# Optimization experiments

Measured on AMD Instinct MI355X. Metric: run time of the kernel, lower is better.

Reference implementation:

```python
import jax, jax.numpy as jnp
import numpy as np

def setup_inputs() -> dict:
    key = jax.random.key(0)
    k1, k2, k3, k4, k5 = jax.random.split(key, 5)
    vocab, embed, hidden = 32000, 1024, 1024
    batch, src_len = 64, 512
    src = jax.random.randint(k1, (batch, src_len), 0, vocab)
    emb_table = jax.random.normal(k2, (vocab, embed), dtype=jnp.float32)
    # xavier_uniform bounds
    bx = float(np.sqrt(6.0 / (embed + hidden)))
    bh = float(np.sqrt(6.0 / (hidden + hidden)))
    W_xh = jax.random.uniform(k3, (hidden, embed), minval=-bx, maxval=bx, dtype=jnp.float32)
    b_xh = jax.random.uniform(k4, (hidden,), minval=-1.0/np.sqrt(embed), maxval=1.0/np.sqrt(embed), dtype=jnp.float32)
    W_hh = jax.random.uniform(k5, (hidden, hidden), minval=-bh, maxval=bh, dtype=jnp.float32)
    return {"src": src, "emb_table": emb_table, "W_xh": W_xh, "b_xh": b_xh, "W_hh": W_hh}

def reference(src, emb_table, W_xh, b_xh, W_hh):
    # embedded: (batch, src_len, embed)
    embedded = emb_table[src]
    # precompute input projection for all timesteps: (batch, src_len, hidden)
    x_proj = jnp.einsum('bte,he->bth', embedded, W_xh) + b_xh
    batch = src.shape[0]
    hidden = W_hh.shape[0]
    h0 = jnp.zeros((batch, hidden), dtype=jnp.float32)

    def step(h, x_t):
        h_new = jnp.tanh(x_t + h @ W_hh.T)
        return h_new, None

    # scan over time: x_proj transposed to (src_len, batch, hidden)
    h_final, _ = jax.lax.scan(step, h0, jnp.swapaxes(x_proj, 0, 1))
    return h_final
```

## Files before the change

### kernel.cpp

```cpp
#include <hip/hip_runtime.h>
#include <hip/hip_fp16.h>

typedef _Float16 half8 __attribute__((ext_vector_type(8)));
typedef float floatx4 __attribute__((ext_vector_type(4)));

#define HBUF_BYTES (2ull * 16 * 1024 * 8)
#define CTL_BYTES  (32ull * 1024)
#define XP_OFF     (HBUF_BYTES + CTL_BYTES)
#define XP_BYTES   (512ull * 64 * 1024 * 2)

#define TAG_BIT    (1ull << 14)

union pack4 { unsigned long long u; _Float16 h[4]; };

__device__ inline half8 cvt8(const float4 a, const float4 b) {
    half8 r;
    r[0] = (_Float16)a.x; r[1] = (_Float16)a.y; r[2] = (_Float16)a.z; r[3] = (_Float16)a.w;
    r[4] = (_Float16)b.x; r[5] = (_Float16)b.y; r[6] = (_Float16)b.z; r[7] = (_Float16)b.w;
    return r;
}

__global__ __launch_bounds__(256) void xproj_kernel(
    const int* __restrict__ src, const float* __restrict__ emb,
    const float* __restrict__ Wxh, const float* __restrict__ bxh,
    _Float16* __restrict__ xp)
{
    __shared__ _Float16 As[128][40];
    __shared__ _Float16 Bs[128][40];

    const int tid  = threadIdx.x;
    const int lane = tid & 63;
    const int w    = tid >> 6;
    const int m15  = lane & 15;
    const int quad = lane >> 4;
    const int bid  = blockIdx.x;
    const int bn   = bid & 7;
    const int bm   = bid >> 3;
    const int m0   = bm * 128, n0 = bn * 128;
    const int wm   = w & 1, wn = w >> 1;

    const int  srow = tid >> 1;
    const int  scol = (tid & 1) * 16;
    const long arow = (long)src[m0 + srow] * 1024;
    const float* abase = emb + arow + scol;
    const float* bbase = Wxh + (long)(n0 + srow) * 1024 + scol;

    floatx4 zero4 = {0.f, 0.f, 0.f, 0.f};
    floatx4 acc[4][4];
#pragma unroll
    for (int mt = 0; mt < 4; mt++)
#pragma unroll
        for (int nt = 0; nt < 4; nt++) acc[mt][nt] = zero4;

    for (int k0 = 0; k0 < 1024; k0 += 32) {
        __syncthreads();
        float4 a0 = *(const float4*)(abase + k0);
        float4 a1 = *(const float4*)(abase + k0 + 4);
        float4 a2 = *(const float4*)(abase + k0 + 8);
        float4 a3 = *(const float4*)(abase + k0 + 12);
        float4 b0 = *(const float4*)(bbase + k0);
        float4 b1 = *(const float4*)(bbase + k0 + 4);
        float4 b2 = *(const float4*)(bbase + k0 + 8);
        float4 b3 = *(const float4*)(bbase + k0 + 12);
        *(half8*)&As[srow][scol]     = cvt8(a0, a1);
        *(half8*)&As[srow][scol + 8] = cvt8(a2, a3);
        *(half8*)&Bs[srow][scol]     = cvt8(b0, b1);
        *(half8*)&Bs[srow][scol + 8] = cvt8(b2, b3);
        __syncthreads();

        half8 af[4], bf[4];
#pragma unroll
        for (int mt = 0; mt < 4; mt++)
            af[mt] = *(const half8*)&As[wm * 64 + mt * 16 + m15][quad * 8];
#pragma unroll
        for (int nt = 0; nt < 4; nt++)
            bf[nt] = *(const half8*)&Bs[wn * 64 + nt * 16 + m15][quad * 8];
#pragma unroll
        for (int mt = 0; mt < 4; mt++)
#pragma unroll
            for (int nt = 0; nt < 4; nt++)
                acc[mt][nt] = __builtin_amdgcn_mfma_f32_16x16x32_f16(
                    af[mt], bf[nt], acc[mt][nt], 0, 0, 0);
    }

#pragma unroll
    for (int nt = 0; nt < 4; nt++) {
        const int n = n0 + wn * 64 + nt * 16 + m15;
        const float bias = bxh[n];
#pragma unroll
        for (int mt = 0; mt < 4; mt++) {
            const int mrow = m0 + wm * 64 + mt * 16 + quad * 4;
#pragma unroll
            for (int r = 0; r < 4; r++) {
                const int m = mrow + r;
                const int b = m >> 9;
                const int t = m & 511;
                xp[((long)t * 64 + b) * 1024 + n] = (_Float16)(acc[mt][nt][r] + bias);
            }
        }
    }
}

__global__ __launch_bounds__(256, 1) void rnn_kernel(
    const float* __restrict__ Whh, const _Float16* __restrict__ xp,
    unsigned long long* __restrict__ hb, float* __restrict__ out)
{
    __shared__ _Float16 hstage[16][1032];
    __shared__ floatx4  cred[4][4][64];

    const int tid    = threadIdx.x;
    const int lane   = tid & 63;
    const int w      = tid >> 6;
    const int m15    = lane & 15;
    const int quad   = lane >> 4;
    const int wg     = blockIdx.x;
    const int g      = wg & 15;
    const int member = wg >> 4;
    const int b0     = g * 4;

    for (int i = tid; i < 16 * 1032; i += 256) ((_Float16*)hstage)[i] = (_Float16)0.f;

    half8 Wf[4][8];
#pragma unroll
    for (int nt = 0; nt < 4; nt++) {
        const float* wrow = Whh + (long)(member * 64 + nt * 16 + m15) * 1024
                                + w * 256 + quad * 8;
#pragma unroll
        for (int kk = 0; kk < 8; kk++) {
            float4 lo = *(const float4*)(wrow + kk * 32);
            float4 hi = *(const float4*)(wrow + kk * 32 + 4);
            Wf[nt][kk] = cvt8(lo, hi);
        }
    }
    __syncthreads();

    const int dim = member * 64 + w * 16 + m15;
    float xv[4] = {0.f, 0.f, 0.f, 0.f};
    if (quad == 0) {
#pragma unroll
        for (int r = 0; r < 4; r++)
            xv[r] = (float)xp[((long)0 * 64 + b0 + r) * 1024 + dim];
    }

    floatx4 zero4 = {0.f, 0.f, 0.f, 0.f};

    for (int t = 0; t < 512; t++) {
        const unsigned long long* hcu = hb + (size_t)(t & 1) * 16384 + (size_t)g * 1024;
        unsigned long long*       hnu = hb + (size_t)((t + 1) & 1) * 16384 + (size_t)g * 1024;
        const unsigned long long exp_tag = (unsigned long long)(((t + 1) >> 1) & 1) << 14;

        unsigned long long v[4];
        for (;;) {
            bool ok = true;
#pragma unroll
            for (int i = 0; i < 4; i++)
                v[i] = __hip_atomic_load(hcu + tid + 256 * i, __ATOMIC_RELAXED,
                                         __HIP_MEMORY_SCOPE_AGENT);
#pragma unroll
            for (int i = 0; i < 4; i++)
                ok &= ((v[i] & TAG_BIT) == exp_tag);
            if (ok) break;
        }
#pragma unroll
        for (int i = 0; i < 4; i++) {
            pack4 p; p.u = v[i] & ~TAG_BIT;
            const int d = tid + 256 * i;
#pragma unroll
            for (int b = 0; b < 4; b++) hstage[b][d] = p.h[b];
        }
        __syncthreads();

        floatx4 pacc[4];
#pragma unroll
        for (int nt = 0; nt < 4; nt++) pacc[nt] = zero4;
#pragma unroll
        for (int kk = 0; kk < 8; kk++) {
            half8 a = *(const half8*)&hstage[m15][w * 256 + kk * 32 + quad * 8];
#pragma unroll
            for (int nt = 0; nt < 4; nt++)
                pacc[nt] = __builtin_amdgcn_mfma_f32_16x16x32_f16(
                    a, Wf[nt][kk], pacc[nt], 0, 0, 0);
        }

#pragma unroll
        for (int nt = 0; nt < 4; nt++) cred[w][nt][lane] = pacc[nt];
        __syncthreads();
        floatx4 dsum = cred[0][w][lane];
#pragma unroll
        for (int ww = 1; ww < 4; ww++) dsum += cred[ww][w][lane];

        if (quad == 0) {
            pack4 p;
#pragma unroll
            for (int r = 0; r < 4; r++) {
                float pre  = dsum[r] + xv[r];
                float e    = __expf(2.0f * pre);
                float hval = 1.0f - 2.0f / (e + 1.0f);
                p.h[r] = (_Float16)hval;
                if (t == 511) out[(b0 + r) * 1024 + dim] = hval;
            }
            if (t < 511) {
                const unsigned long long st_tag =
                    (unsigned long long)(((t + 2) >> 1) & 1) << 14;
                __hip_atomic_store(hnu + dim, p.u | st_tag, __ATOMIC_RELAXED,
                                   __HIP_MEMORY_SCOPE_AGENT);
            }
        }

        if (t < 511 && quad == 0) {
#pragma unroll
            for (int r = 0; r < 4; r++)
                xv[r] = (float)xp[((long)(t + 1) * 64 + b0 + r) * 1024 + dim];
        }
    }
}

extern "C" void kernel_launch(void* const* d_in, const int* in_sizes, int n_in,
                              void* d_out, int out_size, void* d_ws, size_t ws_size,
                              hipStream_t stream) {
    const int*   src = (const int*)d_in[0];
    const float* emb = (const float*)d_in[1];
    const float* Wxh = (const float*)d_in[2];
    const float* bxh = (const float*)d_in[3];
    const float* Whh = (const float*)d_in[4];
    float* out = (float*)d_out;

    char* ws = (char*)d_ws;
    unsigned long long* hb = (unsigned long long*)ws;
    _Float16* xp = (_Float16*)(ws + XP_OFF);

    hipMemsetAsync(ws, 0, HBUF_BYTES, stream);

    hipLaunchKernelGGL(xproj_kernel, dim3(2048), dim3(256), 0, stream,
                       src, emb, Wxh, bxh, xp);

    hipLaunchKernelGGL(rnn_kernel, dim3(256), dim3(256), 0, stream,
                       Whh, xp, hb, out);
}
```

Before: 1.197 ms.

## Give each wave full K per output tile, double-buffer h staging, drop cross-wave reduction

Each wave now owns one 16-column output tile and holds all 32 K-slices of W_hh in registers, so the per-step LDS cross-wave reduction and its extra barrier go away. The hidden-state staging buffer is double-buffered, and the poll for the next step's h moves to the end of the loop, cutting barriers to one per step. The poll also skips reloading entries already seen with the right tag. In exchange each wave carries more weight registers and runs a longer serial chain of MFMAs per step, split over two accumulators.

```diff
diff --git a/kernel.cpp b/kernel.cpp
--- a/kernel.cpp
+++ b/kernel.cpp
@@ -105,8 +105,7 @@
     const float* __restrict__ Whh, const _Float16* __restrict__ xp,
     unsigned long long* __restrict__ hb, float* __restrict__ out)
 {
-    __shared__ _Float16 hstage[16][1032];
-    __shared__ floatx4  cred[4][4][64];
+    __shared__ _Float16 hstage[2][16][1032];
 
     const int tid    = threadIdx.x;
     const int lane   = tid & 63;
@@ -118,18 +117,16 @@
     const int member = wg >> 4;
     const int b0     = g * 4;
 
-    for (int i = tid; i < 16 * 1032; i += 256) ((_Float16*)hstage)[i] = (_Float16)0.f;
-
-    half8 Wf[4][8];
-#pragma unroll
-    for (int nt = 0; nt < 4; nt++) {
-        const float* wrow = Whh + (long)(member * 64 + nt * 16 + m15) * 1024
-                                + w * 256 + quad * 8;
-#pragma unroll
-        for (int kk = 0; kk < 8; kk++) {
+    for (int i = tid; i < 2 * 16 * 1032; i += 256) ((_Float16*)hstage)[i] = (_Float16)0.f;
+
+    half8 Wf[32];
+    {
+        const float* wrow = Whh + (long)(member * 64 + w * 16 + m15) * 1024 + quad * 8;
+#pragma unroll
+        for (int kk = 0; kk < 32; kk++) {
             float4 lo = *(const float4*)(wrow + kk * 32);
             float4 hi = *(const float4*)(wrow + kk * 32 + 4);
-            Wf[nt][kk] = cvt8(lo, hi);
+            Wf[kk] = cvt8(lo, hi);
         }
     }
     __syncthreads();
@@ -145,49 +142,18 @@
     floatx4 zero4 = {0.f, 0.f, 0.f, 0.f};
 
     for (int t = 0; t < 512; t++) {
-        const unsigned long long* hcu = hb + (size_t)(t & 1) * 16384 + (size_t)g * 1024;
-        unsigned long long*       hnu = hb + (size_t)((t + 1) & 1) * 16384 + (size_t)g * 1024;
-        const unsigned long long exp_tag = (unsigned long long)(((t + 1) >> 1) & 1) << 14;
-
-        unsigned long long v[4];
-        for (;;) {
-            bool ok = true;
-#pragma unroll
-            for (int i = 0; i < 4; i++)
-                v[i] = __hip_atomic_load(hcu + tid + 256 * i, __ATOMIC_RELAXED,
-                                         __HIP_MEMORY_SCOPE_AGENT);
-#pragma unroll
-            for (int i = 0; i < 4; i++)
-                ok &= ((v[i] & TAG_BIT) == exp_tag);
-            if (ok) break;
-        }
-#pragma unroll
-        for (int i = 0; i < 4; i++) {
-            pack4 p; p.u = v[i] & ~TAG_BIT;
-            const int d = tid + 256 * i;
-#pragma unroll
-            for (int b = 0; b < 4; b++) hstage[b][d] = p.h[b];
-        }
-        __syncthreads();
-
-        floatx4 pacc[4];
-#pragma unroll
-        for (int nt = 0; nt < 4; nt++) pacc[nt] = zero4;
-#pragma unroll
-        for (int kk = 0; kk < 8; kk++) {
-            half8 a = *(const half8*)&hstage[m15][w * 256 + kk * 32 + quad * 8];
-#pragma unroll
-            for (int nt = 0; nt < 4; nt++)
-                pacc[nt] = __builtin_amdgcn_mfma_f32_16x16x32_f16(
-                    a, Wf[nt][kk], pacc[nt], 0, 0, 0);
-        }
-
-#pragma unroll
-        for (int nt = 0; nt < 4; nt++) cred[w][nt][lane] = pacc[nt];
-        __syncthreads();
-        floatx4 dsum = cred[0][w][lane];
-#pragma unroll
-        for (int ww = 1; ww < 4; ww++) dsum += cred[ww][w][lane];
+        const _Float16 (*cur)[1032] = hstage[t & 1];
+        _Float16       (*nxt)[1032] = hstage[(t + 1) & 1];
+
+        floatx4 acc0 = zero4, acc1 = zero4;
+#pragma unroll
+        for (int kk = 0; kk < 16; kk++) {
+            half8 a0 = *(const half8*)&cur[m15][(2 * kk)     * 32 + quad * 8];
+            half8 a1 = *(const half8*)&cur[m15][(2 * kk + 1) * 32 + quad * 8];
+            acc0 = __builtin_amdgcn_mfma_f32_16x16x32_f16(a0, Wf[2 * kk],     acc0, 0, 0, 0);
+            acc1 = __builtin_amdgcn_mfma_f32_16x16x32_f16(a1, Wf[2 * kk + 1], acc1, 0, 0, 0);
+        }
+        floatx4 dsum = acc0 + acc1;
 
         if (quad == 0) {
             pack4 p;
@@ -200,18 +166,50 @@
                 if (t == 511) out[(b0 + r) * 1024 + dim] = hval;
             }
             if (t < 511) {
+                unsigned long long* hnu =
+                    hb + (size_t)((t + 1) & 1) * 16384 + (size_t)g * 1024;
                 const unsigned long long st_tag =
                     (unsigned long long)(((t + 2) >> 1) & 1) << 14;
                 __hip_atomic_store(hnu + dim, p.u | st_tag, __ATOMIC_RELAXED,
                                    __HIP_MEMORY_SCOPE_AGENT);
             }
         }
-
-        if (t < 511 && quad == 0) {
+        if (t == 511) break;
+
+        if (quad == 0) {
 #pragma unroll
             for (int r = 0; r < 4; r++)
                 xv[r] = (float)xp[((long)(t + 1) * 64 + b0 + r) * 1024 + dim];
         }
+
+        const unsigned long long* hcu =
+            hb + (size_t)((t + 1) & 1) * 16384 + (size_t)g * 1024;
+        const unsigned long long exp_tag =
+            (unsigned long long)(((t + 2) >> 1) & 1) << 14;
+
+        unsigned long long v[4];
+        unsigned okmask = 0;
+        do {
+#pragma unroll
+            for (int i = 0; i < 4; i++)
+                if (!(okmask & (1u << i)))
+                    v[i] = __hip_atomic_load(hcu + tid + 256 * i, __ATOMIC_RELAXED,
+                                             __HIP_MEMORY_SCOPE_AGENT);
+#pragma unroll
+            for (int i = 0; i < 4; i++)
+                if (!(okmask & (1u << i)) && ((v[i] & TAG_BIT) == exp_tag))
+                    okmask |= (1u << i);
+        } while (okmask != 15u);
+
+#pragma unroll
+        for (int i = 0; i < 4; i++) {
+            pack4 p; p.u = v[i] & ~TAG_BIT;
+            const int d = tid + 256 * i;
+#pragma unroll
+            for (int b = 0; b < 4; b++) nxt[b][d] = p.h[b];
+        }
+
+        __syncthreads();
     }
 }
 
```

Result: slower. 1.237 ms (+3.4%).

## Load hidden-state MFMA fragments directly from global with per-element tags, drop LDS staging

Applied to the files above, without the earlier changes.

The recurrent kernel now stores each hidden value as a tagged fp16 in a row-major global buffer. Each lane polls its own MFMA A-fragment straight from global memory, retrying only the 8-byte words whose tags are not yet valid. This removes the LDS staging buffer and one block barrier per timestep, and double-buffers the cross-wave reduction scratch so a second barrier is not needed. The cost is more, finer-grained atomic loads and 2-byte stores. It also depends on the tag bit in each fp16, which overwrites the top exponent bit, and that is only safe because tanh outputs have magnitude at most 1.

```diff
diff --git a/kernel.cpp b/kernel.cpp
--- a/kernel.cpp
+++ b/kernel.cpp
@@ -3,15 +3,18 @@
 
 typedef _Float16 half8 __attribute__((ext_vector_type(8)));
 typedef float floatx4 __attribute__((ext_vector_type(4)));
-
-#define HBUF_BYTES (2ull * 16 * 1024 * 8)
+typedef unsigned long long u64;
+
+#define HBUF_BYTES (2ull * 16 * 4 * 1024 * 2)
 #define CTL_BYTES  (32ull * 1024)
 #define XP_OFF     (HBUF_BYTES + CTL_BYTES)
 #define XP_BYTES   (512ull * 64 * 1024 * 2)
 
-#define TAG_BIT    (1ull << 14)
+#define M8 0x4000400040004000ull
 
 union pack4 { unsigned long long u; _Float16 h[4]; };
+union frag16 { u64 u[2]; half8 h; };
+union h16 { _Float16 h; unsigned short u; };
 
 __device__ inline half8 cvt8(const float4 a, const float4 b) {
     half8 r;
@@ -103,10 +106,9 @@
 
 __global__ __launch_bounds__(256, 1) void rnn_kernel(
     const float* __restrict__ Whh, const _Float16* __restrict__ xp,
-    unsigned long long* __restrict__ hb, float* __restrict__ out)
+    unsigned short* __restrict__ hb, float* __restrict__ out)
 {
-    __shared__ _Float16 hstage[16][1032];
-    __shared__ floatx4  cred[4][4][64];
+    __shared__ floatx4 cred[2][4][4][64];
 
     const int tid    = threadIdx.x;
     const int lane   = tid & 63;
@@ -118,8 +120,6 @@
     const int member = wg >> 4;
     const int b0     = g * 4;
 
-    for (int i = tid; i < 16 * 1032; i += 256) ((_Float16*)hstage)[i] = (_Float16)0.f;
-
     half8 Wf[4][8];
 #pragma unroll
     for (int nt = 0; nt < 4; nt++) {
@@ -132,7 +132,6 @@
             Wf[nt][kk] = cvt8(lo, hi);
         }
     }
-    __syncthreads();
 
     const int dim = member * 64 + w * 16 + m15;
     float xv[4] = {0.f, 0.f, 0.f, 0.f};
@@ -142,68 +141,80 @@
             xv[r] = (float)xp[((long)0 * 64 + b0 + r) * 1024 + dim];
     }
 
+    const unsigned myoff = (unsigned)(g * 4096 + m15 * 1024 + w * 256 + quad * 8);
+
     floatx4 zero4 = {0.f, 0.f, 0.f, 0.f};
+    u64 av[8][2] = {};
 
     for (int t = 0; t < 512; t++) {
-        const unsigned long long* hcu = hb + (size_t)(t & 1) * 16384 + (size_t)g * 1024;
-        unsigned long long*       hnu = hb + (size_t)((t + 1) & 1) * 16384 + (size_t)g * 1024;
-        const unsigned long long exp_tag = (unsigned long long)(((t + 1) >> 1) & 1) << 14;
-
-        unsigned long long v[4];
-        for (;;) {
-            bool ok = true;
-#pragma unroll
-            for (int i = 0; i < 4; i++)
-                v[i] = __hip_atomic_load(hcu + tid + 256 * i, __ATOMIC_RELAXED,
-                                         __HIP_MEMORY_SCOPE_AGENT);
-#pragma unroll
-            for (int i = 0; i < 4; i++)
-                ok &= ((v[i] & TAG_BIT) == exp_tag);
-            if (ok) break;
-        }
-#pragma unroll
-        for (int i = 0; i < 4; i++) {
-            pack4 p; p.u = v[i] & ~TAG_BIT;
-            const int d = tid + 256 * i;
-#pragma unroll
-            for (int b = 0; b < 4; b++) hstage[b][d] = p.h[b];
-        }
-        __syncthreads();
+        if (t > 0) {
+            const u64* hp = (const u64*)(hb + (size_t)(t & 1) * 65536u) + (myoff >> 2);
+            const u64 expM = (((t >> 1) ^ t) & 1) ? M8 : 0ull;
+            unsigned done = (m15 < 4) ? 0u : 0xFFFFu;
+            while (done != 0xFFFFu) {
+#pragma unroll
+                for (int kk = 0; kk < 8; kk++)
+#pragma unroll
+                    for (int hh = 0; hh < 2; hh++)
+                        if (!(done & (1u << (kk * 2 + hh))))
+                            av[kk][hh] = __hip_atomic_load(
+                                hp + kk * 8 + hh, __ATOMIC_RELAXED,
+                                __HIP_MEMORY_SCOPE_AGENT);
+#pragma unroll
+                for (int kk = 0; kk < 8; kk++)
+#pragma unroll
+                    for (int hh = 0; hh < 2; hh++)
+                        if (!(done & (1u << (kk * 2 + hh))) &&
+                            ((av[kk][hh] & M8) == expM))
+                            done |= (1u << (kk * 2 + hh));
+            }
+        }
+
+        half8 a[8];
+#pragma unroll
+        for (int kk = 0; kk < 8; kk++) {
+            frag16 f;
+            f.u[0] = av[kk][0] & ~M8;
+            f.u[1] = av[kk][1] & ~M8;
+            a[kk] = f.h;
+        }
 
         floatx4 pacc[4];
 #pragma unroll
         for (int nt = 0; nt < 4; nt++) pacc[nt] = zero4;
 #pragma unroll
-        for (int kk = 0; kk < 8; kk++) {
-            half8 a = *(const half8*)&hstage[m15][w * 256 + kk * 32 + quad * 8];
+        for (int kk = 0; kk < 8; kk++)
 #pragma unroll
             for (int nt = 0; nt < 4; nt++)
                 pacc[nt] = __builtin_amdgcn_mfma_f32_16x16x32_f16(
-                    a, Wf[nt][kk], pacc[nt], 0, 0, 0);
-        }
-
-#pragma unroll
-        for (int nt = 0; nt < 4; nt++) cred[w][nt][lane] = pacc[nt];
+                    a[kk], Wf[nt][kk], pacc[nt], 0, 0, 0);
+
+        const int cb = t & 1;
+#pragma unroll
+        for (int nt = 0; nt < 4; nt++) cred[cb][w][nt][lane] = pacc[nt];
         __syncthreads();
-        floatx4 dsum = cred[0][w][lane];
-#pragma unroll
-        for (int ww = 1; ww < 4; ww++) dsum += cred[ww][w][lane];
+        floatx4 dsum = cred[cb][0][w][lane];
+#pragma unroll
+        for (int ww = 1; ww < 4; ww++) dsum += cred[cb][ww][w][lane];
 
         if (quad == 0) {
-            pack4 p;
+            const unsigned short tag16 =
+                (unsigned short)((((((t + 1) >> 1) ^ (t + 1)) & 1)) << 14);
+            unsigned short* hs = hb + (size_t)((t + 1) & 1) * 65536u
+                                    + (unsigned)(g * 4096 + dim);
 #pragma unroll
             for (int r = 0; r < 4; r++) {
                 float pre  = dsum[r] + xv[r];
                 float e    = __expf(2.0f * pre);
                 float hval = 1.0f - 2.0f / (e + 1.0f);
-                p.h[r] = (_Float16)hval;
-                if (t == 511) out[(b0 + r) * 1024 + dim] = hval;
-            }
-            if (t < 511) {
-                const unsigned long long st_tag =
-                    (unsigned long long)(((t + 2) >> 1) & 1) << 14;
-                __hip_atomic_store(hnu + dim, p.u | st_tag, __ATOMIC_RELAXED,
-                                   __HIP_MEMORY_SCOPE_AGENT);
+                if (t == 511) {
+                    out[(b0 + r) * 1024 + dim] = hval;
+                } else {
+                    h16 c; c.h = (_Float16)hval;
+                    __hip_atomic_store(hs + r * 1024,
+                                       (unsigned short)(c.u | tag16),
+                                       __ATOMIC_RELAXED, __HIP_MEMORY_SCOPE_AGENT);
+                }
             }
         }
 
@@ -226,7 +237,7 @@
     float* out = (float*)d_out;
 
     char* ws = (char*)d_ws;
-    unsigned long long* hb = (unsigned long long*)ws;
+    unsigned short* hb = (unsigned short*)ws;
     _Float16* xp = (_Float16*)(ws + XP_OFF);
 
     hipMemsetAsync(ws, 0, HBUF_BYTES, stream);
```

Measured after the change: 2.081 ms. +73.9%, slower.

## Drop per-step barrier in RNN loop and prefetch GEMM tiles into registers

Applied to the files above, without the earlier changes.

In the recurrent kernel, each wave now polls and stages only the 256-column k-slice of the hidden state that it consumes itself. That removes the workgroup barrier between staging and the MFMA loop. The cross-wave reduction buffer is double-buffered on timestep parity, so one barrier per step is enough, which shortens the serial per-step critical path. In the input-projection GEMM, the next k-tile's global loads are issued into registers before the MFMAs run, overlapping load latency with compute at the cost of extra registers.

```diff
diff --git a/kernel.cpp b/kernel.cpp
--- a/kernel.cpp
+++ b/kernel.cpp
@@ -3,6 +3,7 @@
 
 typedef _Float16 half8 __attribute__((ext_vector_type(8)));
 typedef float floatx4 __attribute__((ext_vector_type(4)));
+typedef unsigned long long u64;
 
 #define HBUF_BYTES (2ull * 16 * 1024 * 8)
 #define CTL_BYTES  (32ull * 1024)
@@ -52,22 +53,34 @@
 #pragma unroll
         for (int nt = 0; nt < 4; nt++) acc[mt][nt] = zero4;
 
+    float4 a0 = *(const float4*)(abase);
+    float4 a1 = *(const float4*)(abase + 4);
+    float4 a2 = *(const float4*)(abase + 8);
+    float4 a3 = *(const float4*)(abase + 12);
+    float4 b0 = *(const float4*)(bbase);
+    float4 b1 = *(const float4*)(bbase + 4);
+    float4 b2 = *(const float4*)(bbase + 8);
+    float4 b3 = *(const float4*)(bbase + 12);
+
     for (int k0 = 0; k0 < 1024; k0 += 32) {
-        __syncthreads();
-        float4 a0 = *(const float4*)(abase + k0);
-        float4 a1 = *(const float4*)(abase + k0 + 4);
-        float4 a2 = *(const float4*)(abase + k0 + 8);
-        float4 a3 = *(const float4*)(abase + k0 + 12);
-        float4 b0 = *(const float4*)(bbase + k0);
-        float4 b1 = *(const float4*)(bbase + k0 + 4);
-        float4 b2 = *(const float4*)(bbase + k0 + 8);
-        float4 b3 = *(const float4*)(bbase + k0 + 12);
         *(half8*)&As[srow][scol]     = cvt8(a0, a1);
         *(half8*)&As[srow][scol + 8] = cvt8(a2, a3);
         *(half8*)&Bs[srow][scol]     = cvt8(b0, b1);
         *(half8*)&Bs[srow][scol + 8] = cvt8(b2, b3);
         __syncthreads();
 
+        if (k0 + 32 < 1024) {
+            const int kn = k0 + 32;
+            a0 = *(const float4*)(abase + kn);
+            a1 = *(const float4*)(abase + kn + 4);
+            a2 = *(const float4*)(abase + kn + 8);
+            a3 = *(const float4*)(abase + kn + 12);
+            b0 = *(const float4*)(bbase + kn);
+            b1 = *(const float4*)(bbase + kn + 4);
+            b2 = *(const float4*)(bbase + kn + 8);
+            b3 = *(const float4*)(bbase + kn + 12);
+        }
+
         half8 af[4], bf[4];
 #pragma unroll
         for (int mt = 0; mt < 4; mt++)
@@ -81,6 +94,8 @@
             for (int nt = 0; nt < 4; nt++)
                 acc[mt][nt] = __builtin_amdgcn_mfma_f32_16x16x32_f16(
                     af[mt], bf[nt], acc[mt][nt], 0, 0, 0);
+
+        __syncthreads();
     }
 
 #pragma unroll
@@ -106,7 +121,7 @@
     unsigned long long* __restrict__ hb, float* __restrict__ out)
 {
     __shared__ _Float16 hstage[16][1032];
-    __shared__ floatx4  cred[4][4][64];
+    __shared__ floatx4  cred[2][4][4][64];
 
     const int tid    = threadIdx.x;
     const int lane   = tid & 63;
@@ -145,30 +160,30 @@
     floatx4 zero4 = {0.f, 0.f, 0.f, 0.f};
 
     for (int t = 0; t < 512; t++) {
-        const unsigned long long* hcu = hb + (size_t)(t & 1) * 16384 + (size_t)g * 1024;
-        unsigned long long*       hnu = hb + (size_t)((t + 1) & 1) * 16384 + (size_t)g * 1024;
-        const unsigned long long exp_tag = (unsigned long long)(((t + 1) >> 1) & 1) << 14;
-
-        unsigned long long v[4];
+        const u64* hcu = hb + (size_t)(t & 1) * 16384 + (size_t)g * 1024
+                            + (size_t)w * 256;
+        const u64 exp_tag = (u64)(((t + 1) >> 1) & 1) << 14;
+
+        u64 v[4];
         for (;;) {
             bool ok = true;
 #pragma unroll
             for (int i = 0; i < 4; i++)
-                v[i] = __hip_atomic_load(hcu + tid + 256 * i, __ATOMIC_RELAXED,
+                v[i] = __hip_atomic_load(hcu + lane + 64 * i, __ATOMIC_RELAXED,
                                          __HIP_MEMORY_SCOPE_AGENT);
 #pragma unroll
             for (int i = 0; i < 4; i++)
                 ok &= ((v[i] & TAG_BIT) == exp_tag);
             if (ok) break;
         }
+
 #pragma unroll
         for (int i = 0; i < 4; i++) {
             pack4 p; p.u = v[i] & ~TAG_BIT;
-            const int d = tid + 256 * i;
+            const int d = w * 256 + lane + 64 * i;
 #pragma unroll
             for (int b = 0; b < 4; b++) hstage[b][d] = p.h[b];
         }
-        __syncthreads();
 
         floatx4 pacc[4];
 #pragma unroll
@@ -182,12 +197,13 @@
                     a, Wf[nt][kk], pacc[nt], 0, 0, 0);
         }
 
-#pragma unroll
-        for (int nt = 0; nt < 4; nt++) cred[w][nt][lane] = pacc[nt];
+        const int cb = t & 1;
+#pragma unroll
+        for (int nt = 0; nt < 4; nt++) cred[cb][w][nt][lane] = pacc[nt];
         __syncthreads();
-        floatx4 dsum = cred[0][w][lane];
-#pragma unroll
-        for (int ww = 1; ww < 4; ww++) dsum += cred[ww][w][lane];
+        floatx4 dsum = cred[cb][0][w][lane];
+#pragma unroll
+        for (int ww = 1; ww < 4; ww++) dsum += cred[cb][ww][w][lane];
 
         if (quad == 0) {
             pack4 p;
@@ -200,8 +216,9 @@
                 if (t == 511) out[(b0 + r) * 1024 + dim] = hval;
             }
             if (t < 511) {
-                const unsigned long long st_tag =
-                    (unsigned long long)(((t + 2) >> 1) & 1) << 14;
+                unsigned long long* hnu =
+                    hb + (size_t)((t + 1) & 1) * 16384 + (size_t)g * 1024;
+                const u64 st_tag = (u64)(((t + 2) >> 1) & 1) << 14;
                 __hip_atomic_store(hnu + dim, p.u | st_tag, __ATOMIC_RELAXED,
                                    __HIP_MEMORY_SCOPE_AGENT);
             }
```

After: 1.177 ms. About the same (-1.7%).
